# Optimization experiments

Hardware: AMD Instinct MI355X
Metric: run time of the kernel (lower is better)

The kernel has to match this reference:

```python
import jax, jax.numpy as jnp
import numpy as np

B, T = 64, 512
V, E, H, L = 100000, 256, 256, 9


def _lstm(x, Wx, Wh, b):
    # x: [B,T,E] -> hs: [B,T,H]; Keras gate order i,f,c,o
    xg = jnp.einsum('bte,eg->btg', x, Wx) + b  # [B,T,4H]
    h0 = jnp.zeros((x.shape[0], Wh.shape[0]), x.dtype)

    def step(carry, xt):
        h, c = carry
        g = xt + h @ Wh
        i, f, gc, o = jnp.split(g, 4, axis=-1)
        c = jax.nn.sigmoid(f) * c + jax.nn.sigmoid(i) * jnp.tanh(gc)
        h = jax.nn.sigmoid(o) * jnp.tanh(c)
        return (h, c), h

    _, hs = jax.lax.scan(step, (h0, h0), jnp.swapaxes(xg, 0, 1))
    return jnp.swapaxes(hs, 0, 1)


def _crf_log_likelihood(logits, tags, seq_len, trans):
    # logits: [B,T,L], tags: [B,T] int, seq_len: [B] int, trans: [L,L]
    Bb, Tt, Ll = logits.shape
    t_idx = jnp.arange(Tt)
    mask = (t_idx[None, :] < seq_len[:, None]).astype(logits.dtype)  # [B,T]
    # gold path score: unary + pairwise transitions
    unary = jnp.take_along_axis(logits, tags[..., None], axis=-1)[..., 0]  # [B,T]
    unary_score = jnp.sum(unary * mask, axis=-1)
    binary = trans[tags[:, :-1], tags[:, 1:]]  # [B,T-1]
    binary_score = jnp.sum(binary * mask[:, 1:], axis=-1)
    score = unary_score + binary_score
    # forward algorithm (log partition)
    alpha0 = logits[:, 0]  # [B,L]
    step_mask = t_idx[1:, None] < seq_len[None, :]  # [T-1,B]

    def step(alpha, xs):
        logit_t, m = xs  # [B,L], [B]
        new = jax.nn.logsumexp(alpha[:, :, None] + trans[None], axis=1) + logit_t
        alpha = jnp.where(m[:, None], new, alpha)
        return alpha, None

    alpha, _ = jax.lax.scan(step, alpha0, (jnp.swapaxes(logits[:, 1:], 0, 1), step_mask))
    log_norm = jax.nn.logsumexp(alpha, axis=-1)  # [B]
    return score - log_norm


def setup_inputs() -> dict:
    key = jax.random.key(0)
    ks = jax.random.split(key, 12)
    s = 0.05
    return {
        'tokens': jax.random.randint(ks[0], (B, T), 0, V),
        'labels': jax.random.randint(ks[1], (B, T), 0, L),
        'emb_table': jax.random.normal(ks[2], (V, E), jnp.float32) * s,
        'Wx_f': jax.random.normal(ks[3], (E, 4 * H), jnp.float32) * s,
        'Wh_f': jax.random.normal(ks[4], (H, 4 * H), jnp.float32) * s,
        'b_f': jnp.zeros((4 * H,), jnp.float32),
        'Wx_b': jax.random.normal(ks[5], (E, 4 * H), jnp.float32) * s,
        'Wh_b': jax.random.normal(ks[6], (H, 4 * H), jnp.float32) * s,
        'b_b': jnp.zeros((4 * H,), jnp.float32),
        'W_dense': jax.random.normal(ks[7], (2 * H, L), jnp.float32) * s,
        'b_dense': jnp.zeros((L,), jnp.float32),
        'trans': jax.random.uniform(ks[8], (L, L), jnp.float32),
    }


def reference(tokens, labels, emb_table, Wx_f, Wh_f, b_f, Wx_b, Wh_b, b_b, W_dense, b_dense, trans):
    # seq_len = count of non-pad (nonzero) tokens, as in the original call()
    seq_len = jnp.sum((tokens != 0).astype(jnp.int32), axis=-1)  # [B]
    emb = emb_table[tokens]  # [B,T,E]  (dropout inactive at inference)
    h_fwd = _lstm(emb, Wx_f, Wh_f, b_f)
    h_bwd = _lstm(emb[:, ::-1], Wx_b, Wh_b, b_b)[:, ::-1]
    enc = jnp.concatenate([h_fwd, h_bwd], axis=-1)  # [B,T,2H]
    logits = enc @ W_dense + b_dense  # [B,T,L]
    ll = _crf_log_likelihood(logits, labels, seq_len, trans)  # [B]
    return logits, seq_len, ll
```

## Files before the change

### kernel.cpp

```cpp
#include <hip/hip_runtime.h>
#include <hip/hip_fp16.h>


typedef unsigned int  uint32;
typedef unsigned short ushort16;
typedef __attribute__((ext_vector_type(8))) short  short8;
typedef __attribute__((ext_vector_type(4))) float  floatx4;
typedef __attribute__((ext_vector_type(2))) _Float16 half2t;

#define BB 64
#define TT 512
#define NT (BB*TT)
#define G4 1024
#define NL 9
#define KR 96
#define KL 32

__device__ inline float bf2f(ushort16 u) {
  return __builtin_bit_cast(float, ((uint32)u) << 16);
}
__device__ inline ushort16 f2bf(float f) {
  uint32 u = __builtin_bit_cast(uint32, f);
  u += 0x7fffu + ((u >> 16) & 1u);
  return (ushort16)(u >> 16);
}
__device__ inline float sigf(float x)  { return 1.0f / (1.0f + __expf(-x)); }
__device__ inline float tanhf_(float x){ return 1.0f - 2.0f / (1.0f + __expf(2.0f * x)); }

__device__ inline float fdot2_(uint32 w, half2t h, float acc) {
  return __builtin_amdgcn_fdot2(__builtin_bit_cast(half2t, w), h, acc, false);
}

__global__ __launch_bounds__(64) void k_seqlen(const int* __restrict__ tokens,
                                               int* __restrict__ slen,
                                               float* __restrict__ out_sl) {
  const int b = blockIdx.x, lane = threadIdx.x;
  int cnt = 0;
  for (int t = lane; t < TT; t += 64) cnt += (tokens[b * TT + t] != 0) ? 1 : 0;
  #pragma unroll
  for (int off = 32; off >= 1; off >>= 1) cnt += __shfl_down(cnt, off, 64);
  if (lane == 0) { slen[b] = cnt; out_sl[b] = (float)cnt; }
}

__global__ __launch_bounds__(256) void k_embed(const int* __restrict__ tokens,
                                               const float* __restrict__ emb,
                                               ushort16* __restrict__ A) {
  const int f = blockIdx.x * 256 + threadIdx.x;
  const int e = f * 4;
  const int row = e >> 8;
  const int col = e & 255;
  const int tok = tokens[row];
  const float4 v = *(const float4*)(emb + (size_t)tok * 256 + col);
  uint32 lo = (uint32)f2bf(v.x) | ((uint32)f2bf(v.y) << 16);
  uint32 hi = (uint32)f2bf(v.z) | ((uint32)f2bf(v.w) << 16);
  *(uint2*)(A + e) = make_uint2(lo, hi);
}

__global__ __launch_bounds__(256) void k_wxprep(const float* __restrict__ Wxf,
                                                const float* __restrict__ Wxb,
                                                ushort16* __restrict__ BT) {
  const int id = blockIdx.x * 256 + threadIdx.x;
  const int c = id >> 8, k = id & 255;
  const float v = (c < G4) ? Wxf[k * G4 + c] : Wxb[k * G4 + (c - G4)];
  BT[c * 256 + k] = f2bf(v);
}

__global__ __launch_bounds__(256) void k_whprep(const float* __restrict__ Wh,
                                                uint32* __restrict__ W2) {
  const int id = blockIdx.x * 256 + threadIdx.x;
  const int k2 = id >> 10, c = id & 1023;
  const float w0 = Wh[(2 * k2) * G4 + c];
  const float w1 = Wh[(2 * k2 + 1) * G4 + c];
  const ushort16 b0 = __builtin_bit_cast(ushort16, (_Float16)w0);
  const ushort16 b1 = __builtin_bit_cast(ushort16, (_Float16)w1);
  W2[id] = ((uint32)b1 << 16) | (uint32)b0;
}

__global__ __launch_bounds__(256) void k_gemm_xg(const ushort16* __restrict__ A,
                                                 const ushort16* __restrict__ BT,
                                                 const float* __restrict__ bias_f,
                                                 const float* __restrict__ bias_b,
                                                 ushort16* __restrict__ xgf,
                                                 ushort16* __restrict__ xgb) {
  __shared__ __align__(16) ushort16 As[64 * 36];
  __shared__ __align__(16) ushort16 Bs[64 * 36];
  const int m0 = blockIdx.x * 64;
  const int n0 = blockIdx.y * 64;
  const int tid = threadIdx.x;
  const int wave = tid >> 6, lane = tid & 63;
  const int lr = tid >> 2;
  const int lc = (tid & 3) * 8;
  const int am = lane & 15, aq = lane >> 4;
  floatx4 acc[4];
  #pragma unroll
  for (int j = 0; j < 4; ++j) acc[j] = (floatx4){0.f, 0.f, 0.f, 0.f};

  for (int k0 = 0; k0 < 256; k0 += 32) {
    const uint4 va = *(const uint4*)(A  + ((m0 + lr) * 256 + k0 + lc));
    const uint4 vb = *(const uint4*)(BT + ((n0 + lr) * 256 + k0 + lc));
    *(uint2*)&As[lr * 36 + lc]     = make_uint2(va.x, va.y);
    *(uint2*)&As[lr * 36 + lc + 4] = make_uint2(va.z, va.w);
    *(uint2*)&Bs[lr * 36 + lc]     = make_uint2(vb.x, vb.y);
    *(uint2*)&Bs[lr * 36 + lc + 4] = make_uint2(vb.z, vb.w);
    __syncthreads();
    union { uint2 u[2]; short8 s; } fa, fb;
    fa.u[0] = *(const uint2*)&As[(wave * 16 + am) * 36 + aq * 8];
    fa.u[1] = *(const uint2*)&As[(wave * 16 + am) * 36 + aq * 8 + 4];
    #pragma unroll
    for (int j = 0; j < 4; ++j) {
      fb.u[0] = *(const uint2*)&Bs[(j * 16 + am) * 36 + aq * 8];
      fb.u[1] = *(const uint2*)&Bs[(j * 16 + am) * 36 + aq * 8 + 4];
      acc[j] = __builtin_amdgcn_mfma_f32_16x16x32_bf16(fa.s, fb.s, acc[j], 0, 0, 0);
    }
    __syncthreads();
  }
  const int orow = m0 + wave * 16 + aq * 4;
  #pragma unroll
  for (int j = 0; j < 4; ++j) {
    const int col = n0 + j * 16 + am;
    const float bv = (col < G4) ? bias_f[col] : bias_b[col - G4];
    #pragma unroll
    for (int r = 0; r < 4; ++r) {
      const float v = acc[j][r] + bv;
      const int row = orow + r;
      if (col < G4) xgf[row * G4 + col] = f2bf(v);
      else          xgb[row * G4 + (col - G4)] = f2bf(v);
    }
  }
}

__global__ __launch_bounds__(512, 2) void k_lstm(const ushort16* __restrict__ xgf,
                                                 const ushort16* __restrict__ xgb,
                                                 const uint32* __restrict__ Whf,
                                                 const uint32* __restrict__ Whb,
                                                 float* __restrict__ enc) {
  __shared__ uint32 WL[KL * 1024];
  __shared__ float gate[1024];
  __shared__ ushort16 h16[2][256];
  const int bi = blockIdx.x;
  const int dir = bi >> 6, b = bi & 63;
  const int tid = threadIdx.x;
  const int w = tid >> 6, l = tid & 63;
  const int colA = w * 128 + l;
  const int colB = colA + 64;
  const ushort16* xg = dir ? xgb : xgf;
  const uint32* W2 = dir ? Whb : Whf;

  for (int idx = tid; idx < KL * 1024; idx += 512) {
    const int k2r = idx >> 10, c = idx & 1023;
    WL[k2r * 1024 + ((c >> 7) << 7) + ((c & 63) << 1) + ((c >> 6) & 1)] =
        W2[(KR + k2r) * 1024 + c];
  }
  uint32 wA[KR], wB[KR];
  #pragma unroll
  for (int i = 0; i < KR; ++i) {
    wA[i] = W2[i * 1024 + colA];
    wB[i] = W2[i * 1024 + colB];
  }
  if (tid < 128) ((uint32*)h16[0])[tid] = 0u;
  float c_state = 0.f;
  __syncthreads();

  for (int s = 0; s < TT; ++s) {
    const int t = dir ? (TT - 1 - s) : s;
    const int row = b * TT + t;
    const ushort16* xr = xg + (size_t)row * G4;
    float acc0 = bf2f(xr[colA]);
    float acc1 = 0.f;
    float acc2 = bf2f(xr[colB]);
    float acc3 = 0.f;
    const uint32* hrd = (const uint32*)h16[s & 1];
    const int hl = l & 31;
    const uint32 hv0 = hrd[hl];
    const uint32 hv1 = hrd[32 + hl];
    const uint32 hv2 = hrd[64 + hl];
    const uint32 hv3 = hrd[96 + hl];
    #pragma unroll
    for (int q = 0; q < 3; ++q) {
      const uint32 hvq = (q == 0) ? hv0 : (q == 1) ? hv1 : hv2;
      #pragma unroll
      for (int i = 0; i < 32; ++i) {
        const half2t hh = __builtin_bit_cast(
            half2t, (uint32)__builtin_amdgcn_readlane((int)hvq, i));
        const int k = q * 32 + i;
        if (i & 1) { acc1 = fdot2_(wA[k], hh, acc1); acc3 = fdot2_(wB[k], hh, acc3); }
        else       { acc0 = fdot2_(wA[k], hh, acc0); acc2 = fdot2_(wB[k], hh, acc2); }
      }
    }
    {
      const uint32* wl = WL + w * 128 + (l << 1);
      #pragma unroll
      for (int i = 0; i < 32; ++i) {
        const half2t hh = __builtin_bit_cast(
            half2t, (uint32)__builtin_amdgcn_readlane((int)hv3, i));
        const uint2 wp = *(const uint2*)(wl + i * 1024);
        if (i & 1) { acc1 = fdot2_(wp.x, hh, acc1); acc3 = fdot2_(wp.y, hh, acc3); }
        else       { acc0 = fdot2_(wp.x, hh, acc0); acc2 = fdot2_(wp.y, hh, acc2); }
      }
    }
    gate[colA] = acc0 + acc1;
    gate[colB] = acc2 + acc3;
    __syncthreads();
    if (tid < 256) {
      const float gi = gate[tid];
      const float gf = gate[256 + tid];
      const float gg = gate[512 + tid];
      const float go = gate[768 + tid];
      c_state = sigf(gf) * c_state + sigf(gi) * tanhf_(gg);
      const float h = sigf(go) * tanhf_(c_state);
      h16[(s + 1) & 1][tid] = __builtin_bit_cast(ushort16, (_Float16)h);
      enc[(size_t)row * 512 + dir * 256 + tid] = h;
    }
    __syncthreads();
  }
}

__global__ __launch_bounds__(256) void k_dense(const float* __restrict__ enc,
                                               const float* __restrict__ Wd,
                                               const float* __restrict__ bd,
                                               float* __restrict__ logits) {
  __shared__ float Wl[512 * NL];
  __shared__ float bl[NL];
  const int tid = threadIdx.x;
  for (int i = tid; i < 512 * NL; i += 256) Wl[i] = Wd[i];
  if (tid < NL) bl[tid] = bd[tid];
  __syncthreads();
  const int wave = tid >> 6, lane = tid & 63;
  const int row = blockIdx.x * 4 + wave;
  const float* er = enc + (size_t)row * 512;
  float p[NL];
  #pragma unroll
  for (int c = 0; c < NL; ++c) p[c] = 0.f;
  #pragma unroll
  for (int u = 0; u < 8; ++u) {
    const int k = u * 64 + lane;
    const float v = er[k];
    const float* wr = &Wl[k * NL];
    #pragma unroll
    for (int c = 0; c < NL; ++c) p[c] += v * wr[c];
  }
  #pragma unroll
  for (int c = 0; c < NL; ++c) {
    #pragma unroll
    for (int off = 32; off >= 1; off >>= 1) p[c] += __shfl_down(p[c], off, 64);
  }
  if (lane == 0) {
    float* orow = logits + (size_t)row * NL;
    #pragma unroll
    for (int c = 0; c < NL; ++c) orow[c] = p[c] + bl[c];
  }
}

__global__ __launch_bounds__(64) void k_crf(const float* __restrict__ logits,
                                            const int* __restrict__ labels,
                                            const int* __restrict__ slen,
                                            const float* __restrict__ trans,
                                            float* __restrict__ out_ll) {
  __shared__ float tr[NL * NL];
  __shared__ float alpha[NL];
  const int b = blockIdx.x;
  const int lane = threadIdx.x;
  for (int i = lane; i < NL * NL; i += 64) tr[i] = trans[i];
  __syncthreads();
  const int len = slen[b];
  const int* tg = labels + b * TT;
  const float* lg = logits + (size_t)b * TT * NL;
  float s = 0.f;
  for (int t = lane; t < TT; t += 64)
    if (t < len) s += lg[t * NL + tg[t]];
  for (int t = lane; t < TT - 1; t += 64)
    if (t + 1 < len) s += tr[tg[t] * NL + tg[t + 1]];
  #pragma unroll
  for (int off = 32; off >= 1; off >>= 1) s += __shfl_down(s, off, 64);
  if (lane < NL) alpha[lane] = lg[lane];
  __syncthreads();
  if (lane < NL) {
    const int j = lane;
    for (int t = 1; t < TT; ++t) {
      if (t < len) {
        float av[NL];
        float m = -1e30f;
        #pragma unroll
        for (int i = 0; i < NL; ++i) { av[i] = alpha[i] + tr[i * NL + j]; m = fmaxf(m, av[i]); }
        float ss = 0.f;
        #pragma unroll
        for (int i = 0; i < NL; ++i) ss += __expf(av[i] - m);
        const float nj = m + __logf(ss) + lg[t * NL + j];
        alpha[j] = nj;
      }
    }
  }
  __syncthreads();
  if (lane == 0) {
    float m = -1e30f;
    #pragma unroll
    for (int i = 0; i < NL; ++i) m = fmaxf(m, alpha[i]);
    float ss = 0.f;
    #pragma unroll
    for (int i = 0; i < NL; ++i) ss += __expf(alpha[i] - m);
    out_ll[b] = s - (m + __logf(ss));
  }
}

extern "C" void kernel_launch(void* const* d_in, const int* in_sizes, int n_in,
                              void* d_out, int out_size, void* d_ws, size_t ws_size,
                              hipStream_t stream) {
  (void)in_sizes; (void)n_in; (void)out_size; (void)ws_size;
  const int*   tokens = (const int*)d_in[0];
  const int*   labels = (const int*)d_in[1];
  const float* emb    = (const float*)d_in[2];
  const float* Wxf    = (const float*)d_in[3];
  const float* Whf    = (const float*)d_in[4];
  const float* bf_    = (const float*)d_in[5];
  const float* Wxb    = (const float*)d_in[6];
  const float* Whb    = (const float*)d_in[7];
  const float* bb_    = (const float*)d_in[8];
  const float* Wd     = (const float*)d_in[9];
  const float* bd     = (const float*)d_in[10];
  const float* trans  = (const float*)d_in[11];
  float* out = (float*)d_out;

  char* ws = (char*)d_ws;
  ushort16* A    = (ushort16*)(ws + 0);
  ushort16* BT   = (ushort16*)(ws + 16777216);
  uint32*   W2f  = (uint32*)  (ws + 17825792);
  uint32*   W2b  = (uint32*)  (ws + 18350080);
  ushort16* xgf  = (ushort16*)(ws + 18874368);
  ushort16* xgb  = (ushort16*)(ws + 85983232);
  float*    enc  = (float*)   (ws + 153092096);
  int*      slen = (int*)     (ws + 220200960);

  k_seqlen<<<BB, 64, 0, stream>>>(tokens, slen, out + NT * NL);
  k_embed <<<NT * 256 / 4 / 256, 256, 0, stream>>>(tokens, emb, A);
  k_wxprep<<<2048 * 256 / 256, 256, 0, stream>>>(Wxf, Wxb, BT);
  k_whprep<<<128 * 1024 / 256, 256, 0, stream>>>(Whf, W2f);
  k_whprep<<<128 * 1024 / 256, 256, 0, stream>>>(Whb, W2b);
  k_gemm_xg<<<dim3(NT / 64, 2048 / 64), 256, 0, stream>>>(A, BT, bf_, bb_, xgf, xgb);
  k_lstm  <<<128, 512, 0, stream>>>(xgf, xgb, W2f, W2b, enc);
  k_dense <<<NT / 4, 256, 0, stream>>>(enc, Wd, bd, out);
  k_crf   <<<BB, 64, 0, stream>>>(out, labels, slen, trans, out + NT * NL + BB);
}
```

Baseline: 1.487 ms.

## Broadcast h via LDS vector loads, prefetch next-step xg, rebalance register/LDS weight split

In the LSTM recurrence kernel, each lane now reads the hidden state as uint4 broadcast loads from LDS instead of readlane across wave lanes. The next timestep's input-gate values are loaded during the current step, hiding global-load latency behind the dot products. The split between register-held and LDS-held recurrent weights moves from 96/32 to 92/36, with an asm barrier pinning the register copies, and the LDS weight layout becomes per-wave contiguous. The packed fp16 h is built with a lane shuffle; the risks are register pressure and extra LDS traffic.

```diff
diff --git a/kernel.cpp b/kernel.cpp
--- a/kernel.cpp
+++ b/kernel.cpp
@@ -13,8 +13,8 @@
 #define NT (BB*TT)
 #define G4 1024
 #define NL 9
-#define KR 96
-#define KL 32
+#define KR 92
+#define KL 36
 
 __device__ inline float bf2f(ushort16 u) {
   return __builtin_bit_cast(float, ((uint32)u) << 16);
@@ -136,7 +136,7 @@
                                                  float* __restrict__ enc) {
   __shared__ uint32 WL[KL * 1024];
   __shared__ float gate[1024];
-  __shared__ ushort16 h16[2][256];
+  __shared__ __align__(16) uint32 h2buf[2][128];
   const int bi = blockIdx.x;
   const int dir = bi >> 6, b = bi & 63;
   const int tid = threadIdx.x;
@@ -148,7 +148,7 @@
 
   for (int idx = tid; idx < KL * 1024; idx += 512) {
     const int k2r = idx >> 10, c = idx & 1023;
-    WL[k2r * 1024 + ((c >> 7) << 7) + ((c & 63) << 1) + ((c >> 6) & 1)] =
+    WL[(c >> 7) * (KL * 128) + k2r * 128 + ((c & 63) << 1) + ((c >> 6) & 1)] =
         W2[(KR + k2r) * 1024 + c];
   }
   uint32 wA[KR], wB[KR];
@@ -157,45 +157,48 @@
     wA[i] = W2[i * 1024 + colA];
     wB[i] = W2[i * 1024 + colB];
   }
-  if (tid < 128) ((uint32*)h16[0])[tid] = 0u;
+  #pragma unroll
+  for (int i = 0; i < KR; ++i) asm volatile("" : "+v"(wA[i]), "+v"(wB[i]));
+
+  if (tid < 128) h2buf[0][tid] = 0u;
   float c_state = 0.f;
   __syncthreads();
 
+  const uint32* wl = WL + w * (KL * 128) + (l << 1);
+  {
+  }
+  const int t0 = dir ? (TT - 1) : 0;
+  ushort16 xA = xg[(size_t)(b * TT + t0) * G4 + colA];
+  ushort16 xB = xg[(size_t)(b * TT + t0) * G4 + colB];
+
   for (int s = 0; s < TT; ++s) {
-    const int t = dir ? (TT - 1 - s) : s;
-    const int row = b * TT + t;
-    const ushort16* xr = xg + (size_t)row * G4;
-    float acc0 = bf2f(xr[colA]);
+    float acc0 = bf2f(xA);
     float acc1 = 0.f;
-    float acc2 = bf2f(xr[colB]);
+    float acc2 = bf2f(xB);
     float acc3 = 0.f;
-    const uint32* hrd = (const uint32*)h16[s & 1];
-    const int hl = l & 31;
-    const uint32 hv0 = hrd[hl];
-    const uint32 hv1 = hrd[32 + hl];
-    const uint32 hv2 = hrd[64 + hl];
-    const uint32 hv3 = hrd[96 + hl];
-    #pragma unroll
-    for (int q = 0; q < 3; ++q) {
-      const uint32 hvq = (q == 0) ? hv0 : (q == 1) ? hv1 : hv2;
+    if (s + 1 < TT) {
+      const int t1 = dir ? (TT - 2 - s) : (s + 1);
+      const ushort16* xr1 = xg + (size_t)(b * TT + t1) * G4;
+      xA = xr1[colA];
+      xB = xr1[colB];
+    }
+    const uint4* hb = (const uint4*)h2buf[s & 1];
+    #pragma unroll
+    for (int blk = 0; blk < 32; ++blk) {
+      const uint4 hq = hb[blk];
       #pragma unroll
-      for (int i = 0; i < 32; ++i) {
-        const half2t hh = __builtin_bit_cast(
-            half2t, (uint32)__builtin_amdgcn_readlane((int)hvq, i));
-        const int k = q * 32 + i;
-        if (i & 1) { acc1 = fdot2_(wA[k], hh, acc1); acc3 = fdot2_(wB[k], hh, acc3); }
-        else       { acc0 = fdot2_(wA[k], hh, acc0); acc2 = fdot2_(wB[k], hh, acc2); }
-      }
-    }
-    {
-      const uint32* wl = WL + w * 128 + (l << 1);
-      #pragma unroll
-      for (int i = 0; i < 32; ++i) {
-        const half2t hh = __builtin_bit_cast(
-            half2t, (uint32)__builtin_amdgcn_readlane((int)hv3, i));
-        const uint2 wp = *(const uint2*)(wl + i * 1024);
-        if (i & 1) { acc1 = fdot2_(wp.x, hh, acc1); acc3 = fdot2_(wp.y, hh, acc3); }
-        else       { acc0 = fdot2_(wp.x, hh, acc0); acc2 = fdot2_(wp.y, hh, acc2); }
+      for (int j = 0; j < 4; ++j) {
+        const int k2 = blk * 4 + j;
+        const uint32 hu = (j == 0) ? hq.x : (j == 1) ? hq.y : (j == 2) ? hq.z : hq.w;
+        const half2t hh = __builtin_bit_cast(half2t, hu);
+        if (k2 < KR) {
+          if (j & 1) { acc1 = fdot2_(wA[k2], hh, acc1); acc3 = fdot2_(wB[k2], hh, acc3); }
+          else       { acc0 = fdot2_(wA[k2], hh, acc0); acc2 = fdot2_(wB[k2], hh, acc2); }
+        } else {
+          const uint2 wp = *(const uint2*)(wl + (k2 - KR) * 128);
+          if (j & 1) { acc1 = fdot2_(wp.x, hh, acc1); acc3 = fdot2_(wp.y, hh, acc3); }
+          else       { acc0 = fdot2_(wp.x, hh, acc0); acc2 = fdot2_(wp.y, hh, acc2); }
+        }
       }
     }
     gate[colA] = acc0 + acc1;
@@ -208,8 +211,12 @@
       const float go = gate[768 + tid];
       c_state = sigf(gf) * c_state + sigf(gi) * tanhf_(gg);
       const float h = sigf(go) * tanhf_(c_state);
-      h16[(s + 1) & 1][tid] = __builtin_bit_cast(ushort16, (_Float16)h);
+      const int row = b * TT + (dir ? (TT - 1 - s) : s);
       enc[(size_t)row * 512 + dir * 256 + tid] = h;
+      const int hv = (int)(uint32)__builtin_bit_cast(ushort16, (_Float16)h);
+      const int ho = __shfl_xor(hv, 1, 64);
+      if (!(tid & 1))
+        h2buf[(s + 1) & 1][tid >> 1] = ((uint32)hv & 0xffffu) | ((uint32)ho << 16);
     }
     __syncthreads();
   }
```

Result: faster. 1.403 ms (-5.7%).
